# Performance work log

Hardware: AMD Instinct MI355X
Metric: run time of the kernel (lower is better)

## Reference

```python
import jax, jax.numpy as jnp
import numpy as np

NEG_INF = -1e9
LN_EPS = 1e-5

N, F_IN, F_OUT, H = 4096, 128, 64, 4


def setup_inputs() -> dict:
    key = jax.random.key(0)
    ks = jax.random.split(key, 8)
    return {
        "nodes_features": jax.random.normal(ks[0], (N, F_IN), jnp.float32),
        "degree_matrix": jax.random.normal(ks[1], (N, N), jnp.float32),
        "edges_features_distance": jax.random.normal(ks[2], (N, N), jnp.float32),
        "edges_features_bond": jax.random.normal(ks[3], (N, N), jnp.float32),
        "proj_param": jax.random.normal(ks[4], (H, F_IN, F_OUT), jnp.float32) * 0.1,
        "score_src": jax.random.normal(ks[5], (H, F_OUT, 1), jnp.float32) * 0.1,
        "score_tgt": jax.random.normal(ks[6], (H, F_OUT, 1), jnp.float32) * 0.1,
        "skip_w": jax.random.normal(ks[7], (H * F_OUT, F_IN), jnp.float32) * 0.1,
        "cutoff": 0,
    }


def reference(nodes_features, degree_matrix, edges_features_distance,
              edges_features_bond, proj_param, score_src, score_tgt,
              skip_w, cutoff):
    # connectivity mask: nested where on degree/bond matrices  [N, N]
    wdm = degree_matrix + edges_features_bond
    mask = jnp.where(wdm > 0, wdm,
                     jnp.where(edges_features_bond > cutoff,
                               edges_features_bond + wdm, NEG_INF))

    # per-head projection: [H, N, F_out]
    proj = jnp.einsum('nf,hfo->hno', nodes_features, proj_param)

    # scalar scores per node per head: [H, N, 1]
    s_src = jnp.einsum('hno,hop->hnp', proj, score_src)
    s_tgt = jnp.einsum('hno,hop->hnp', proj, score_tgt)

    # broadcast score matrix [H, N, N]; softmax over dim=1 (as in the original)
    scores = jax.nn.leaky_relu(s_src + jnp.swapaxes(s_tgt, 1, 2), negative_slope=0.2)
    attn = jax.nn.softmax(scores + mask[None, :, :], axis=1)

    # weighted aggregation: [H, N, F_out] -> [N, H, F_out]
    out = jnp.einsum('hij,hjf->hif', attn, proj)
    out = jnp.swapaxes(out, 0, 1)

    # skip connection (F_in != F_out -> linear skip projection)
    skip = (nodes_features @ skip_w.T).reshape(-1, H, F_OUT)
    out = out + skip

    # concat heads, ELU activation (no bias: ctor passes bias=None)
    out = jax.nn.elu(out.reshape(-1, H * F_OUT))

    # fresh LayerNorm (weight=1, bias=0) over last dim of mask
    mu = jnp.mean(mask, axis=-1, keepdims=True)
    var = jnp.var(mask, axis=-1, keepdims=True)
    mask_ln = (mask - mu) / jnp.sqrt(var + LN_EPS)

    return out, mask_ln
```

## Files before the change

### kernel.cpp

```cpp
#include <hip/hip_runtime.h>
#include <math.h>

constexpr int kN  = 4096;
constexpr int kFI = 128;
constexpr int kFO = 64;
constexpr int kH  = 4;
constexpr int kHF = 256;
constexpr float kNegInf = -1e9f;
constexpr float kLnEps  = 1e-5f;
constexpr float kL2E    = 1.44269504f;

typedef short bf16x8 __attribute__((ext_vector_type(8)));
typedef float f32x4  __attribute__((ext_vector_type(4)));

__device__ __forceinline__ float wave_sum(float v){
  #pragma unroll
  for (int s = 32; s > 0; s >>= 1) v += __shfl_xor(v, s, 64);
  return v;
}

__device__ __forceinline__ unsigned short f2bf(float x){
  unsigned u = __float_as_uint(x);
  u = (u + 0x7fffu + ((u >> 16) & 1u)) >> 16;
  return (unsigned short)u;
}
__device__ __forceinline__ unsigned f2bf_pk(float a, float b){
  return (unsigned)f2bf(a) | ((unsigned)f2bf(b) << 16);
}

__global__ __launch_bounds__(256) void k_tr(
    const float* __restrict__ skw, float* __restrict__ skwT)
{
  const int k  = blockIdx.x;
  const int hf = threadIdx.x;
  skwT[k*kHF + hf] = skw[hf*kFI + k];
}

__global__ __launch_bounds__(256) void k_proj(
    const float* __restrict__ nodes, const float* __restrict__ pp,
    const float* __restrict__ ssrc,  const float* __restrict__ stgt,
    const float* __restrict__ skwT,
    float* __restrict__ proj, float* __restrict__ ga, float* __restrict__ gb,
    float* __restrict__ skipo)
{
  __shared__ float feat[8][kFI];
  const int tid = threadIdx.x;
  const int n0  = blockIdx.x * 8;
  for (int idx = tid; idx < 8*kFI; idx += 256)
    feat[idx >> 7][idx & 127] = nodes[n0*kFI + idx];
  __syncthreads();
  const int h = tid >> 6, o = tid & 63;
  float accP[8], accS[8];
  #pragma unroll
  for (int n = 0; n < 8; ++n){ accP[n] = 0.f; accS[n] = 0.f; }
  for (int k0 = 0; k0 < kFI; k0 += 4){
    float p[4], w[4];
    #pragma unroll
    for (int u = 0; u < 4; ++u){
      p[u] = pp[(h*kFI + k0+u)*kFO + o];
      w[u] = skwT[(k0+u)*kHF + tid];
    }
    #pragma unroll
    for (int n = 0; n < 8; ++n){
      const float4 f4 = *(const float4*)&feat[n][k0];
      accP[n] = fmaf(f4.x, p[0], fmaf(f4.y, p[1],
                fmaf(f4.z, p[2], fmaf(f4.w, p[3], accP[n]))));
      accS[n] = fmaf(f4.x, w[0], fmaf(f4.y, w[1],
                fmaf(f4.z, w[2], fmaf(f4.w, w[3], accS[n]))));
    }
  }
  const float sa = ssrc[h*kFO + o];
  const float sb = stgt[h*kFO + o];
  #pragma unroll
  for (int n = 0; n < 8; ++n){
    proj[(h*kN + n0+n)*kFO + o] = accP[n];
    skipo[(n0+n)*kHF + tid]     = accS[n];
    const float va = wave_sum(accP[n] * sa);
    const float vb = wave_sum(accP[n] * sb);
    if (o == 0){ ga[h*kN + n0+n] = va; gb[h*kN + n0+n] = vb; }
  }
}

template<int RS>
__global__ __launch_bounds__(256) void k_colsum(
    const float* __restrict__ degm, const float* __restrict__ bondm,
    const float* __restrict__ ga,   const float* __restrict__ gb,
    const int* __restrict__ cutp,
    float* __restrict__ Spart, float* __restrict__ statg)
{
  const int j0 = (blockIdx.x * 256 + threadIdx.x) * 4;
  const int lane = threadIdx.x & 63;
  const float cut = (float)cutp[0];
  float4 bv[kH]; f32x4 sv[kH];
  #pragma unroll
  for (int h = 0; h < kH; ++h){
    bv[h] = *(const float4*)&gb[h*kN + j0];
    sv[h] = (f32x4){0.f, 0.f, 0.f, 0.f};
  }
  float msum[RS], msq[RS];
  #pragma unroll
  for (int r = 0; r < RS; ++r){ msum[r] = 0.f; msq[r] = 0.f; }

  const int i0 = blockIdx.y * RS;
  #pragma unroll
  for (int ib = 0; ib < RS; ib += 8){
    float4 dg[8], bd[8];
    #pragma unroll
    for (int u = 0; u < 8; ++u){
      const size_t off = (size_t)(i0+ib+u)*kN + j0;
      dg[u] = *(const float4*)&degm[off];
      bd[u] = *(const float4*)&bondm[off];
    }
    #pragma unroll
    for (int u = 0; u < 8; ++u){
      const int i = i0 + ib + u;
      float4 m;
      {
        float w0 = dg[u].x + bd[u].x, w1 = dg[u].y + bd[u].y;
        float w2 = dg[u].z + bd[u].z, w3 = dg[u].w + bd[u].w;
        m.x = w0 > 0.f ? w0 : (bd[u].x > cut ? bd[u].x + w0 : kNegInf);
        m.y = w1 > 0.f ? w1 : (bd[u].y > cut ? bd[u].y + w1 : kNegInf);
        m.z = w2 > 0.f ? w2 : (bd[u].z > cut ? bd[u].z + w2 : kNegInf);
        m.w = w3 > 0.f ? w3 : (bd[u].w > cut ? bd[u].w + w3 : kNegInf);
      }
      msum[ib+u] += (m.x + m.y) + (m.z + m.w);
      msq[ib+u]  += fmaf(m.x, m.x, fmaf(m.y, m.y, fmaf(m.z, m.z, m.w*m.w)));
      const float4 ml = {m.x*kL2E, m.y*kL2E, m.z*kL2E, m.w*kL2E};
      #pragma unroll
      for (int h = 0; h < kH; ++h){
        const float a = ga[h*kN + i];
        float t0 = a + bv[h].x, t1 = a + bv[h].y;
        float t2 = a + bv[h].z, t3 = a + bv[h].w;
        t0 = fmaxf(t0, 0.2f*t0); t1 = fmaxf(t1, 0.2f*t1);
        t2 = fmaxf(t2, 0.2f*t2); t3 = fmaxf(t3, 0.2f*t3);
        sv[h][0] += exp2f(fmaf(t0, kL2E, ml.x));
        sv[h][1] += exp2f(fmaf(t1, kL2E, ml.y));
        sv[h][2] += exp2f(fmaf(t2, kL2E, ml.z));
        sv[h][3] += exp2f(fmaf(t3, kL2E, ml.w));
      }
    }
  }
  #pragma unroll
  for (int h = 0; h < kH; ++h)
    *(float4*)&Spart[(size_t)(blockIdx.y*kH + h)*kN + j0] = *(float4*)&sv[h];

  #pragma unroll
  for (int r = 0; r < RS; ++r){
    const float s1 = wave_sum(msum[r]);
    const float s2 = wave_sum(msq[r]);
    if (lane == 0){
      atomicAdd(&statg[2*(i0+r)+0], s1);
      atomicAdd(&statg[2*(i0+r)+1], s2);
    }
  }
}

__global__ __launch_bounds__(256) void k_sred(
    const float* __restrict__ Spart, float* __restrict__ S, int strips)
{
  __shared__ float red[4][64];
  const int hj0  = blockIdx.x * 64;
  const int lane = threadIdx.x & 63;
  const int g    = threadIdx.x >> 6;
  const int per_chunk = strips >> 3;
  const int per_wave  = per_chunk >> 2;
  const int p0 = blockIdx.y*per_chunk + g*per_wave;
  float s0=0.f, s1=0.f, s2=0.f, s3=0.f;
  for (int p = p0; p < p0 + per_wave; p += 4){
    s0 += Spart[(size_t)(p+0)*kH*kN + hj0 + lane];
    s1 += Spart[(size_t)(p+1)*kH*kN + hj0 + lane];
    s2 += Spart[(size_t)(p+2)*kH*kN + hj0 + lane];
    s3 += Spart[(size_t)(p+3)*kH*kN + hj0 + lane];
  }
  red[g][lane] = (s0+s1)+(s2+s3);
  __syncthreads();
  if (threadIdx.x < 64)
    atomicAdd(&S[hj0+lane],
              (red[0][lane]+red[1][lane])+(red[2][lane]+red[3][lane]));
}

__global__ __launch_bounds__(256) void k_stat(
    const float* __restrict__ statg, float* __restrict__ statg2)
{
  const int i = blockIdx.x * 256 + threadIdx.x;
  const float mu  = statg[2*i] * (1.f/kN);
  const float var = statg[2*i+1] * (1.f/kN) - mu*mu;
  statg2[2*i+0] = mu;
  statg2[2*i+1] = rsqrtf(var + kLnEps);
}

__global__ __launch_bounds__(256) void k_pack(
    const float* __restrict__ proj, const float* __restrict__ S,
    unsigned short* __restrict__ pSpack)
{
  const int t = blockIdx.x * 256 + threadIdx.x;
  const int L  = t & 63;
  const int nt = (t >> 6) & 3;
  const int kb = (t >> 8) & 127;
  const int h  = t >> 15;
  const int f  = nt*16 + (L & 15);
  const int jb = kb*32 + (L >> 4)*8;
  union { unsigned short s[8]; uint4 v; } u;
  #pragma unroll
  for (int r = 0; r < 8; ++r){
    const int j = jb + r;
    u.s[r] = f2bf(proj[(size_t)(h*kN + j)*kFO + f] / S[h*kN + j]);
  }
  ((uint4*)pSpack)[t] = u.v;
}

__global__ __launch_bounds__(256) void k_aggr(
    const float* __restrict__ degm, const float* __restrict__ bondm,
    const float* __restrict__ ga, const float* __restrict__ gb,
    const int* __restrict__ cutp,
    const unsigned short* __restrict__ pSpack,
    const float* __restrict__ statg2,
    float* __restrict__ accpart, float* __restrict__ mlnp, int span)
{
  const int tid  = threadIdx.x;
  const int w    = tid >> 6;
  const int L    = tid & 63;
  const int rbase= blockIdx.x*64 + w*16;
  const int row  = rbase + (L & 15);
  const int colg = (L >> 4) * 8;
  const int jq   = blockIdx.y;
  const int jq0  = jq * span;
  const int nchunk = span >> 5;
  const float cut = (float)cutp[0];

  const float mu = statg2[2*row+0];
  const float rs = statg2[2*row+1];
  float av[kH];
  #pragma unroll
  for (int h = 0; h < kH; ++h) av[h] = ga[h*kN + row];

  f32x4 acc[kH][4];
  #pragma unroll
  for (int h = 0; h < kH; ++h)
    #pragma unroll
    for (int nt = 0; nt < 4; ++nt) acc[h][nt] = (f32x4){0.f,0.f,0.f,0.f};

  const size_t rowbase = (size_t)row * kN;

  float4 dg0 = *(const float4*)&degm[rowbase + jq0 + colg];
  float4 dg1 = *(const float4*)&degm[rowbase + jq0 + colg + 4];
  float4 bd0 = *(const float4*)&bondm[rowbase + jq0 + colg];
  float4 bd1 = *(const float4*)&bondm[rowbase + jq0 + colg + 4];

  for (int c = 0; c < nchunk; ++c){
    const int cb = jq0 + (c << 5);
    float4 ndg0 = dg0, ndg1 = dg1, nbd0 = bd0, nbd1 = bd1;
    if (c+1 < nchunk){
      const size_t noff = rowbase + cb + 32 + colg;
      ndg0 = *(const float4*)&degm[noff];
      ndg1 = *(const float4*)&degm[noff + 4];
      nbd0 = *(const float4*)&bondm[noff];
      nbd1 = *(const float4*)&bondm[noff + 4];
    }

    const float dgv[8] = {dg0.x,dg0.y,dg0.z,dg0.w, dg1.x,dg1.y,dg1.z,dg1.w};
    const float bdv[8] = {bd0.x,bd0.y,bd0.z,bd0.w, bd1.x,bd1.y,bd1.z,bd1.w};
    float m[8], ml[8];
    #pragma unroll
    for (int r = 0; r < 8; ++r){
      const float wv = dgv[r] + bdv[r];
      m[r]  = wv > 0.f ? wv : (bdv[r] > cut ? bdv[r] + wv : kNegInf);
      ml[r] = m[r] * kL2E;
    }
    {
      float4 o0, o1;
      o0.x = (m[0]-mu)*rs; o0.y = (m[1]-mu)*rs;
      o0.z = (m[2]-mu)*rs; o0.w = (m[3]-mu)*rs;
      o1.x = (m[4]-mu)*rs; o1.y = (m[5]-mu)*rs;
      o1.z = (m[6]-mu)*rs; o1.w = (m[7]-mu)*rs;
      *(float4*)&mlnp[rowbase + cb + colg]     = o0;
      *(float4*)&mlnp[rowbase + cb + colg + 4] = o1;
    }
    const int kb = cb >> 5;
    #pragma unroll
    for (int h = 0; h < kH; ++h){
      const float4 g0 = *(const float4*)&gb[h*kN + cb + colg];
      const float4 g1 = *(const float4*)&gb[h*kN + cb + colg + 4];
      const float gv[8] = {g0.x,g0.y,g0.z,g0.w, g1.x,g1.y,g1.z,g1.w};
      union { unsigned u[4]; bf16x8 v; } ua;
      #pragma unroll
      for (int r2 = 0; r2 < 4; ++r2){
        float t0 = av[h] + gv[2*r2],   t1 = av[h] + gv[2*r2+1];
        t0 = fmaxf(t0, 0.2f*t0);       t1 = fmaxf(t1, 0.2f*t1);
        const float e0 = exp2f(fmaf(t0, kL2E, ml[2*r2]));
        const float e1 = exp2f(fmaf(t1, kL2E, ml[2*r2+1]));
        ua.u[r2] = f2bf_pk(e0, e1);
      }
      #pragma unroll
      for (int nt = 0; nt < 4; ++nt){
        const bf16x8 b = *(const bf16x8*)&pSpack[(size_t)(((h*128 + kb)*4 + nt)*64 + L)*8];
        acc[h][nt] = __builtin_amdgcn_mfma_f32_16x16x32_bf16(ua.v, b, acc[h][nt], 0, 0, 0);
      }
    }
    dg0 = ndg0; dg1 = ndg1; bd0 = nbd0; bd1 = nbd1;
  }

  #pragma unroll
  for (int h = 0; h < kH; ++h)
    #pragma unroll
    for (int nt = 0; nt < 4; ++nt)
      #pragma unroll
      for (int reg = 0; reg < 4; ++reg){
        const int i = rbase + (L >> 4)*4 + reg;
        const int f = h*64 + nt*16 + (L & 15);
        accpart[((size_t)jq*kN + i)*kHF + f] = acc[h][nt][reg];
      }
}

__global__ __launch_bounds__(256) void k_out(
    const float* __restrict__ accpart, const float* __restrict__ skipo,
    float* __restrict__ outp, int nq)
{
  const int idx = blockIdx.x * 256 + threadIdx.x;
  float o = skipo[idx];
  for (int q = 0; q < nq; ++q) o += accpart[(size_t)q*kN*kHF + idx];
  o = o > 0.f ? o : expm1f(o);
  outp[idx] = o;
}

extern "C" void kernel_launch(void* const* d_in, const int* in_sizes, int n_in,
                              void* d_out, int out_size, void* d_ws, size_t ws_size,
                              hipStream_t stream)
{
  const float* nodes = (const float*)d_in[0];
  const float* degm  = (const float*)d_in[1];
  const float* bondm = (const float*)d_in[3];
  const float* pp    = (const float*)d_in[4];
  const float* ssrc  = (const float*)d_in[5];
  const float* stgt  = (const float*)d_in[6];
  const float* skw   = (const float*)d_in[7];
  const int*   cutp  = (const int*)d_in[8];

  const size_t fixed_floats = (size_t)kH*kN*kFO + 3*(size_t)kH*kN
                            + (size_t)kN*kHF + 4*(size_t)kN + (size_t)kFI*kHF;
  const size_t psp_floats = ((size_t)kH*kN*kFO)/2;
  const size_t need16 = (fixed_floats + (size_t)16*kN*kHF + psp_floats)*sizeof(float);
  const size_t need8  = (fixed_floats + (size_t)8*kN*kHF  + psp_floats)*sizeof(float);

  int nq, strips;
  if      (ws_size >= need16){ nq = 16; strips = 512; }
  else if (ws_size >= need8) { nq = 8;  strips = 512; }
  else                       { nq = 4;  strips = 256; }

  float* ws     = (float*)d_ws;
  float* proj   = ws;
  float* ga     = proj + (size_t)kH*kN*kFO;
  float* gb     = ga + kH*kN;
  float* statg  = gb + kH*kN;
  float* statg2 = statg + 2*kN;
  float* S      = statg2 + 2*kN;
  float* skip   = S + kH*kN;
  float* skwT   = skip + (size_t)kN*kHF;
  float* accpart= skwT + (size_t)kFI*kHF;
  float* Spart  = accpart;
  unsigned short* pSpack = (unsigned short*)(accpart + (size_t)nq*kN*kHF);

  float* outp = (float*)d_out;
  float* mlnp = outp + (size_t)kN*kHF;

  hipMemsetAsync(statg, 0, (4*(size_t)kN + (size_t)kH*kN)*sizeof(float), stream);

  k_tr<<<kFI, 256, 0, stream>>>(skw, skwT);
  k_proj<<<kN/8, 256, 0, stream>>>(nodes, pp, ssrc, stgt, skwT, proj, ga, gb, skip);
  if (strips == 512)
    k_colsum<8><<<dim3(kN/1024, 512), 256, 0, stream>>>(degm, bondm, ga, gb, cutp,
                                                        Spart, statg);
  else
    k_colsum<16><<<dim3(kN/1024, 256), 256, 0, stream>>>(degm, bondm, ga, gb, cutp,
                                                         Spart, statg);
  k_sred<<<dim3((kH*kN)/64, 8), 256, 0, stream>>>(Spart, S, strips);
  k_stat<<<kN/256, 256, 0, stream>>>(statg, statg2);
  k_pack<<<(kH*128*4*64)/256, 256, 0, stream>>>(proj, S, pSpack);
  k_aggr<<<dim3(kN/64, nq), 256, 0, stream>>>(degm, bondm, ga, gb, cutp,
                                              pSpack, statg2, accpart, mlnp,
                                              kN/nq);
  k_out<<<(kN*kHF)/256, 256, 0, stream>>>(accpart, skip, outp, nq);
}
```

Measured before the change: 331.2 us.

## Fold softmax normalization into exponent and fuse pack, stats, and reductions

Instead of dividing proj by the column sums S in a separate pack kernel, k_proj now writes bf16 MFMA-packed proj directly and k_aggr subtracts log2(S) inside the exponent. k_colsum accumulates S with global atomics rather than writing partials reduced by k_sred. k_stat is folded into k_aggr and the skip-weight transpose kernel is dropped. The goal is fewer launches and less intermediate traffic, at the cost of more atomic contention on S, an extra log per element in k_aggr, and a fixed split of 8 instead of choosing 16 from workspace size.

```diff
diff --git a/kernel.cpp b/kernel.cpp
--- a/kernel.cpp
+++ b/kernel.cpp
@@ -6,6 +6,7 @@
 constexpr int kFO = 64;
 constexpr int kH  = 4;
 constexpr int kHF = 256;
+constexpr int kNQ = 8;
 constexpr float kNegInf = -1e9f;
 constexpr float kLnEps  = 1e-5f;
 constexpr float kL2E    = 1.44269504f;
@@ -28,20 +29,12 @@
   return (unsigned)f2bf(a) | ((unsigned)f2bf(b) << 16);
 }
 
-__global__ __launch_bounds__(256) void k_tr(
-    const float* __restrict__ skw, float* __restrict__ skwT)
-{
-  const int k  = blockIdx.x;
-  const int hf = threadIdx.x;
-  skwT[k*kHF + hf] = skw[hf*kFI + k];
-}
-
 __global__ __launch_bounds__(256) void k_proj(
     const float* __restrict__ nodes, const float* __restrict__ pp,
     const float* __restrict__ ssrc,  const float* __restrict__ stgt,
-    const float* __restrict__ skwT,
-    float* __restrict__ proj, float* __restrict__ ga, float* __restrict__ gb,
-    float* __restrict__ skipo)
+    const float* __restrict__ skw,
+    unsigned short* __restrict__ pSpack, float* __restrict__ ga,
+    float* __restrict__ gb, float* __restrict__ skipo)
 {
   __shared__ float feat[8][kFI];
   const int tid = threadIdx.x;
@@ -54,39 +47,46 @@
   #pragma unroll
   for (int n = 0; n < 8; ++n){ accP[n] = 0.f; accS[n] = 0.f; }
   for (int k0 = 0; k0 < kFI; k0 += 4){
-    float p[4], w[4];
-    #pragma unroll
-    for (int u = 0; u < 4; ++u){
+    float p[4];
+    const float4 w4 = *(const float4*)&skw[tid*kFI + k0];
+    #pragma unroll
+    for (int u = 0; u < 4; ++u)
       p[u] = pp[(h*kFI + k0+u)*kFO + o];
-      w[u] = skwT[(k0+u)*kHF + tid];
-    }
     #pragma unroll
     for (int n = 0; n < 8; ++n){
       const float4 f4 = *(const float4*)&feat[n][k0];
       accP[n] = fmaf(f4.x, p[0], fmaf(f4.y, p[1],
                 fmaf(f4.z, p[2], fmaf(f4.w, p[3], accP[n]))));
-      accS[n] = fmaf(f4.x, w[0], fmaf(f4.y, w[1],
-                fmaf(f4.z, w[2], fmaf(f4.w, w[3], accS[n]))));
+      accS[n] = fmaf(f4.x, w4.x, fmaf(f4.y, w4.y,
+                fmaf(f4.z, w4.z, fmaf(f4.w, w4.w, accS[n]))));
     }
   }
   const float sa = ssrc[h*kFO + o];
   const float sb = stgt[h*kFO + o];
   #pragma unroll
   for (int n = 0; n < 8; ++n){
-    proj[(h*kN + n0+n)*kFO + o] = accP[n];
-    skipo[(n0+n)*kHF + tid]     = accS[n];
+    skipo[(n0+n)*kHF + tid] = accS[n];
     const float va = wave_sum(accP[n] * sa);
     const float vb = wave_sum(accP[n] * sb);
     if (o == 0){ ga[h*kN + n0+n] = va; gb[h*kN + n0+n] = vb; }
   }
-}
-
-template<int RS>
+  {
+    const int kb = n0 >> 5;
+    const int nt = o >> 4;
+    const int L  = (((n0 >> 3) & 3) << 4) | (o & 15);
+    union { unsigned u[4]; uint4 v; } pk;
+    #pragma unroll
+    for (int r2 = 0; r2 < 4; ++r2)
+      pk.u[r2] = f2bf_pk(accP[2*r2], accP[2*r2+1]);
+    ((uint4*)pSpack)[((h*128 + kb)*4 + nt)*64 + L] = pk.v;
+  }
+}
+
 __global__ __launch_bounds__(256) void k_colsum(
     const float* __restrict__ degm, const float* __restrict__ bondm,
     const float* __restrict__ ga,   const float* __restrict__ gb,
     const int* __restrict__ cutp,
-    float* __restrict__ Spart, float* __restrict__ statg)
+    float* __restrict__ S, float* __restrict__ statg)
 {
   const int j0 = (blockIdx.x * 256 + threadIdx.x) * 4;
   const int lane = threadIdx.x & 63;
@@ -97,55 +97,55 @@
     bv[h] = *(const float4*)&gb[h*kN + j0];
     sv[h] = (f32x4){0.f, 0.f, 0.f, 0.f};
   }
-  float msum[RS], msq[RS];
-  #pragma unroll
-  for (int r = 0; r < RS; ++r){ msum[r] = 0.f; msq[r] = 0.f; }
-
-  const int i0 = blockIdx.y * RS;
-  #pragma unroll
-  for (int ib = 0; ib < RS; ib += 8){
-    float4 dg[8], bd[8];
-    #pragma unroll
-    for (int u = 0; u < 8; ++u){
-      const size_t off = (size_t)(i0+ib+u)*kN + j0;
-      dg[u] = *(const float4*)&degm[off];
-      bd[u] = *(const float4*)&bondm[off];
-    }
-    #pragma unroll
-    for (int u = 0; u < 8; ++u){
-      const int i = i0 + ib + u;
-      float4 m;
-      {
-        float w0 = dg[u].x + bd[u].x, w1 = dg[u].y + bd[u].y;
-        float w2 = dg[u].z + bd[u].z, w3 = dg[u].w + bd[u].w;
-        m.x = w0 > 0.f ? w0 : (bd[u].x > cut ? bd[u].x + w0 : kNegInf);
-        m.y = w1 > 0.f ? w1 : (bd[u].y > cut ? bd[u].y + w1 : kNegInf);
-        m.z = w2 > 0.f ? w2 : (bd[u].z > cut ? bd[u].z + w2 : kNegInf);
-        m.w = w3 > 0.f ? w3 : (bd[u].w > cut ? bd[u].w + w3 : kNegInf);
-      }
-      msum[ib+u] += (m.x + m.y) + (m.z + m.w);
-      msq[ib+u]  += fmaf(m.x, m.x, fmaf(m.y, m.y, fmaf(m.z, m.z, m.w*m.w)));
-      const float4 ml = {m.x*kL2E, m.y*kL2E, m.z*kL2E, m.w*kL2E};
-      #pragma unroll
-      for (int h = 0; h < kH; ++h){
-        const float a = ga[h*kN + i];
-        float t0 = a + bv[h].x, t1 = a + bv[h].y;
-        float t2 = a + bv[h].z, t3 = a + bv[h].w;
-        t0 = fmaxf(t0, 0.2f*t0); t1 = fmaxf(t1, 0.2f*t1);
-        t2 = fmaxf(t2, 0.2f*t2); t3 = fmaxf(t3, 0.2f*t3);
-        sv[h][0] += exp2f(fmaf(t0, kL2E, ml.x));
-        sv[h][1] += exp2f(fmaf(t1, kL2E, ml.y));
-        sv[h][2] += exp2f(fmaf(t2, kL2E, ml.z));
-        sv[h][3] += exp2f(fmaf(t3, kL2E, ml.w));
-      }
-    }
-  }
-  #pragma unroll
-  for (int h = 0; h < kH; ++h)
-    *(float4*)&Spart[(size_t)(blockIdx.y*kH + h)*kN + j0] = *(float4*)&sv[h];
-
-  #pragma unroll
-  for (int r = 0; r < RS; ++r){
+  float msum[8], msq[8];
+  #pragma unroll
+  for (int r = 0; r < 8; ++r){ msum[r] = 0.f; msq[r] = 0.f; }
+
+  const int i0 = blockIdx.y * 8;
+  float4 dg[8], bd[8];
+  #pragma unroll
+  for (int u = 0; u < 8; ++u){
+    const size_t off = (size_t)(i0+u)*kN + j0;
+    dg[u] = *(const float4*)&degm[off];
+    bd[u] = *(const float4*)&bondm[off];
+  }
+  #pragma unroll
+  for (int u = 0; u < 8; ++u){
+    const int i = i0 + u;
+    float4 m;
+    {
+      float w0 = dg[u].x + bd[u].x, w1 = dg[u].y + bd[u].y;
+      float w2 = dg[u].z + bd[u].z, w3 = dg[u].w + bd[u].w;
+      m.x = w0 > 0.f ? w0 : (bd[u].x > cut ? bd[u].x + w0 : kNegInf);
+      m.y = w1 > 0.f ? w1 : (bd[u].y > cut ? bd[u].y + w1 : kNegInf);
+      m.z = w2 > 0.f ? w2 : (bd[u].z > cut ? bd[u].z + w2 : kNegInf);
+      m.w = w3 > 0.f ? w3 : (bd[u].w > cut ? bd[u].w + w3 : kNegInf);
+    }
+    msum[u] += (m.x + m.y) + (m.z + m.w);
+    msq[u]  += fmaf(m.x, m.x, fmaf(m.y, m.y, fmaf(m.z, m.z, m.w*m.w)));
+    const float4 ml = {m.x*kL2E, m.y*kL2E, m.z*kL2E, m.w*kL2E};
+    #pragma unroll
+    for (int h = 0; h < kH; ++h){
+      const float a = ga[h*kN + i];
+      float t0 = a + bv[h].x, t1 = a + bv[h].y;
+      float t2 = a + bv[h].z, t3 = a + bv[h].w;
+      t0 = fmaxf(t0, 0.2f*t0); t1 = fmaxf(t1, 0.2f*t1);
+      t2 = fmaxf(t2, 0.2f*t2); t3 = fmaxf(t3, 0.2f*t3);
+      sv[h][0] += exp2f(fmaf(t0, kL2E, ml.x));
+      sv[h][1] += exp2f(fmaf(t1, kL2E, ml.y));
+      sv[h][2] += exp2f(fmaf(t2, kL2E, ml.z));
+      sv[h][3] += exp2f(fmaf(t3, kL2E, ml.w));
+    }
+  }
+  #pragma unroll
+  for (int h = 0; h < kH; ++h){
+    atomicAdd(&S[h*kN + j0 + 0], sv[h][0]);
+    atomicAdd(&S[h*kN + j0 + 1], sv[h][1]);
+    atomicAdd(&S[h*kN + j0 + 2], sv[h][2]);
+    atomicAdd(&S[h*kN + j0 + 3], sv[h][3]);
+  }
+  #pragma unroll
+  for (int r = 0; r < 8; ++r){
     const float s1 = wave_sum(msum[r]);
     const float s2 = wave_sum(msq[r]);
     if (lane == 0){
@@ -155,67 +155,13 @@
   }
 }
 
-__global__ __launch_bounds__(256) void k_sred(
-    const float* __restrict__ Spart, float* __restrict__ S, int strips)
-{
-  __shared__ float red[4][64];
-  const int hj0  = blockIdx.x * 64;
-  const int lane = threadIdx.x & 63;
-  const int g    = threadIdx.x >> 6;
-  const int per_chunk = strips >> 3;
-  const int per_wave  = per_chunk >> 2;
-  const int p0 = blockIdx.y*per_chunk + g*per_wave;
-  float s0=0.f, s1=0.f, s2=0.f, s3=0.f;
-  for (int p = p0; p < p0 + per_wave; p += 4){
-    s0 += Spart[(size_t)(p+0)*kH*kN + hj0 + lane];
-    s1 += Spart[(size_t)(p+1)*kH*kN + hj0 + lane];
-    s2 += Spart[(size_t)(p+2)*kH*kN + hj0 + lane];
-    s3 += Spart[(size_t)(p+3)*kH*kN + hj0 + lane];
-  }
-  red[g][lane] = (s0+s1)+(s2+s3);
-  __syncthreads();
-  if (threadIdx.x < 64)
-    atomicAdd(&S[hj0+lane],
-              (red[0][lane]+red[1][lane])+(red[2][lane]+red[3][lane]));
-}
-
-__global__ __launch_bounds__(256) void k_stat(
-    const float* __restrict__ statg, float* __restrict__ statg2)
-{
-  const int i = blockIdx.x * 256 + threadIdx.x;
-  const float mu  = statg[2*i] * (1.f/kN);
-  const float var = statg[2*i+1] * (1.f/kN) - mu*mu;
-  statg2[2*i+0] = mu;
-  statg2[2*i+1] = rsqrtf(var + kLnEps);
-}
-
-__global__ __launch_bounds__(256) void k_pack(
-    const float* __restrict__ proj, const float* __restrict__ S,
-    unsigned short* __restrict__ pSpack)
-{
-  const int t = blockIdx.x * 256 + threadIdx.x;
-  const int L  = t & 63;
-  const int nt = (t >> 6) & 3;
-  const int kb = (t >> 8) & 127;
-  const int h  = t >> 15;
-  const int f  = nt*16 + (L & 15);
-  const int jb = kb*32 + (L >> 4)*8;
-  union { unsigned short s[8]; uint4 v; } u;
-  #pragma unroll
-  for (int r = 0; r < 8; ++r){
-    const int j = jb + r;
-    u.s[r] = f2bf(proj[(size_t)(h*kN + j)*kFO + f] / S[h*kN + j]);
-  }
-  ((uint4*)pSpack)[t] = u.v;
-}
-
 __global__ __launch_bounds__(256) void k_aggr(
     const float* __restrict__ degm, const float* __restrict__ bondm,
     const float* __restrict__ ga, const float* __restrict__ gb,
     const int* __restrict__ cutp,
     const unsigned short* __restrict__ pSpack,
-    const float* __restrict__ statg2,
-    float* __restrict__ accpart, float* __restrict__ mlnp, int span)
+    const float* __restrict__ statg, const float* __restrict__ S,
+    float* __restrict__ accpart, float* __restrict__ mlnp)
 {
   const int tid  = threadIdx.x;
   const int w    = tid >> 6;
@@ -224,12 +170,14 @@
   const int row  = rbase + (L & 15);
   const int colg = (L >> 4) * 8;
   const int jq   = blockIdx.y;
+  const int span = kN / kNQ;
   const int jq0  = jq * span;
   const int nchunk = span >> 5;
   const float cut = (float)cutp[0];
 
-  const float mu = statg2[2*row+0];
-  const float rs = statg2[2*row+1];
+  const float mu = statg[2*row+0] * (1.f/kN);
+  const float var = statg[2*row+1] * (1.f/kN) - mu*mu;
+  const float rs = rsqrtf(var + kLnEps);
   float av[kH];
   #pragma unroll
   for (int h = 0; h < kH; ++h) av[h] = ga[h*kN + row];
@@ -281,14 +229,20 @@
     for (int h = 0; h < kH; ++h){
       const float4 g0 = *(const float4*)&gb[h*kN + cb + colg];
       const float4 g1 = *(const float4*)&gb[h*kN + cb + colg + 4];
+      const float4 s0 = *(const float4*)&S[h*kN + cb + colg];
+      const float4 s1 = *(const float4*)&S[h*kN + cb + colg + 4];
       const float gv[8] = {g0.x,g0.y,g0.z,g0.w, g1.x,g1.y,g1.z,g1.w};
+      const float sw[8] = {s0.x,s0.y,s0.z,s0.w, s1.x,s1.y,s1.z,s1.w};
+      float mlh[8];
+      #pragma unroll
+      for (int r = 0; r < 8; ++r) mlh[r] = ml[r] - __log2f(sw[r]);
       union { unsigned u[4]; bf16x8 v; } ua;
       #pragma unroll
       for (int r2 = 0; r2 < 4; ++r2){
         float t0 = av[h] + gv[2*r2],   t1 = av[h] + gv[2*r2+1];
         t0 = fmaxf(t0, 0.2f*t0);       t1 = fmaxf(t1, 0.2f*t1);
-        const float e0 = exp2f(fmaf(t0, kL2E, ml[2*r2]));
-        const float e1 = exp2f(fmaf(t1, kL2E, ml[2*r2+1]));
+        const float e0 = exp2f(fmaf(t0, kL2E, mlh[2*r2]));
+        const float e1 = exp2f(fmaf(t1, kL2E, mlh[2*r2+1]));
         ua.u[r2] = f2bf_pk(e0, e1);
       }
       #pragma unroll
@@ -314,11 +268,12 @@
 
 __global__ __launch_bounds__(256) void k_out(
     const float* __restrict__ accpart, const float* __restrict__ skipo,
-    float* __restrict__ outp, int nq)
+    float* __restrict__ outp)
 {
   const int idx = blockIdx.x * 256 + threadIdx.x;
   float o = skipo[idx];
-  for (int q = 0; q < nq; ++q) o += accpart[(size_t)q*kN*kHF + idx];
+  #pragma unroll
+  for (int q = 0; q < kNQ; ++q) o += accpart[(size_t)q*kN*kHF + idx];
   o = o > 0.f ? o : expm1f(o);
   outp[idx] = o;
 }
@@ -336,48 +291,25 @@
   const float* skw   = (const float*)d_in[7];
   const int*   cutp  = (const int*)d_in[8];
 
-  const size_t fixed_floats = (size_t)kH*kN*kFO + 3*(size_t)kH*kN
-                            + (size_t)kN*kHF + 4*(size_t)kN + (size_t)kFI*kHF;
-  const size_t psp_floats = ((size_t)kH*kN*kFO)/2;
-  const size_t need16 = (fixed_floats + (size_t)16*kN*kHF + psp_floats)*sizeof(float);
-  const size_t need8  = (fixed_floats + (size_t)8*kN*kHF  + psp_floats)*sizeof(float);
-
-  int nq, strips;
-  if      (ws_size >= need16){ nq = 16; strips = 512; }
-  else if (ws_size >= need8) { nq = 8;  strips = 512; }
-  else                       { nq = 4;  strips = 256; }
-
   float* ws     = (float*)d_ws;
-  float* proj   = ws;
-  float* ga     = proj + (size_t)kH*kN*kFO;
+  float* ga     = ws;
   float* gb     = ga + kH*kN;
   float* statg  = gb + kH*kN;
-  float* statg2 = statg + 2*kN;
-  float* S      = statg2 + 2*kN;
+  float* S      = statg + 2*kN;
   float* skip   = S + kH*kN;
-  float* skwT   = skip + (size_t)kN*kHF;
-  float* accpart= skwT + (size_t)kFI*kHF;
-  float* Spart  = accpart;
-  unsigned short* pSpack = (unsigned short*)(accpart + (size_t)nq*kN*kHF);
+  float* accpart= skip + (size_t)kN*kHF;
+  unsigned short* pSpack = (unsigned short*)(accpart + (size_t)kNQ*kN*kHF);
 
   float* outp = (float*)d_out;
   float* mlnp = outp + (size_t)kN*kHF;
 
-  hipMemsetAsync(statg, 0, (4*(size_t)kN + (size_t)kH*kN)*sizeof(float), stream);
-
-  k_tr<<<kFI, 256, 0, stream>>>(skw, skwT);
-  k_proj<<<kN/8, 256, 0, stream>>>(nodes, pp, ssrc, stgt, skwT, proj, ga, gb, skip);
-  if (strips == 512)
-    k_colsum<8><<<dim3(kN/1024, 512), 256, 0, stream>>>(degm, bondm, ga, gb, cutp,
-                                                        Spart, statg);
-  else
-    k_colsum<16><<<dim3(kN/1024, 256), 256, 0, stream>>>(degm, bondm, ga, gb, cutp,
-                                                         Spart, statg);
-  k_sred<<<dim3((kH*kN)/64, 8), 256, 0, stream>>>(Spart, S, strips);
-  k_stat<<<kN/256, 256, 0, stream>>>(statg, statg2);
-  k_pack<<<(kH*128*4*64)/256, 256, 0, stream>>>(proj, S, pSpack);
-  k_aggr<<<dim3(kN/64, nq), 256, 0, stream>>>(degm, bondm, ga, gb, cutp,
-                                              pSpack, statg2, accpart, mlnp,
-                                              kN/nq);
-  k_out<<<(kN*kHF)/256, 256, 0, stream>>>(accpart, skip, outp, nq);
-}
+  hipMemsetAsync(statg, 0, (2*(size_t)kN + (size_t)kH*kN)*sizeof(float), stream);
+
+  k_proj<<<kN/8, 256, 0, stream>>>(nodes, pp, ssrc, stgt, skw,
+                                   pSpack, ga, gb, skip);
+  k_colsum<<<dim3(4, kN/8), 256, 0, stream>>>(degm, bondm, ga, gb, cutp,
+                                              S, statg);
+  k_aggr<<<dim3(kN/64, kNQ), 256, 0, stream>>>(degm, bondm, ga, gb, cutp,
+                                               pSpack, statg, S, accpart, mlnp);
+  k_out<<<(kN*kHF)/256, 256, 0, stream>>>(accpart, skip, outp);
+}
```

Measured after the change: 416.0 us. +25.6%, slower.
